# Performance work log

Measured on AMD Instinct MI355X. Metric: run time of the kernel, lower is better.

Reference implementation:

```python
import jax, jax.numpy as jnp
import numpy as np

S, B, E = 128, 64, 512          # seqlen, batch, incoming feature dim
P_LEN, P_DIM = 160, 512         # post length, post_size
H = 1024                        # hidden_size; GRU input_size = E + P_DIM = 1024
NEG = -1000000000.0             # masked_fill value in maskedSoftmax


def setup_inputs() -> dict:
    key = jax.random.key(0)
    ks = jax.random.split(key, 11)
    s = 1.0 / np.sqrt(H)
    u = lambda k, shp: jax.random.uniform(k, shp, jnp.float32, -s, s)
    return {
        "incoming": jax.random.normal(ks[0], (S, B, E), jnp.float32),
        "post": jax.random.normal(ks[1], (P_LEN, B, P_DIM), jnp.float32),
        "h_init": u(ks[2], (1, 1, H)),
        "weight_ih": u(ks[3], (3 * H, E + P_DIM)),
        "weight_hh": u(ks[4], (3 * H, H)),
        "bias_ih": u(ks[5], (3 * H,)),
        "bias_hh": u(ks[6], (3 * H,)),
        "wq": u(ks[7], (P_DIM, H)),
        "bq": u(ks[8], (P_DIM,)),
        "length": jax.random.randint(ks[9], (B,), 1, S + 1),
        "post_length": jax.random.randint(ks[10], (B,), 1, P_LEN + 1),
    }


def reference(incoming, post, h_init, weight_ih, weight_hh, bias_ih, bias_hh,
              wq, bq, length, post_length):
    seqlen, batch = incoming.shape[0], incoming.shape[1]
    plen = post.shape[0]
    h0 = jnp.broadcast_to(h_init[0], (batch, h_init.shape[-1]))  # h_init.repeat(1,B,1)[0]
    pos_mask = jnp.arange(plen)[:, None] < post_length[None, :]  # [P, B]

    def step(h, xt_i):
        xt, i = xt_i
        # attention over post, softmax along post-length axis (dim 0)
        query = h @ wq.T + bq                                   # [B, P_DIM]
        scores = jnp.einsum('pbd,bd->pb', post, query)          # [P, B]
        attn = jax.nn.softmax(jnp.where(pos_mask, scores, NEG), axis=0)
        context = jnp.einsum('pb,pbd->bd', attn, post)          # [B, P_DIM]
        x = jnp.concatenate([xt, context], axis=-1)             # [B, E + P_DIM]
        # torch GRUCell (gate order: r, z, n)
        gi = x @ weight_ih.T + bias_ih                          # [B, 3H]
        gh = h @ weight_hh.T + bias_hh                          # [B, 3H]
        i_r, i_z, i_n = jnp.split(gi, 3, axis=-1)
        h_r, h_z, h_n = jnp.split(gh, 3, axis=-1)
        r = jax.nn.sigmoid(i_r + h_r)
        z = jax.nn.sigmoid(i_z + h_z)
        n = jnp.tanh(i_n + r * h_n)
        h_new = (1.0 - z) * n + z * h
        # zero out finished sequences: h_now * (length > i)
        h_new = h_new * (length > i)[:, None].astype(h.dtype)
        return h_new, h_new

    h_last, hs = jax.lax.scan(step, h0, (incoming, jnp.arange(seqlen)))
    return hs, h_last
```

## Files before the change

kernel.cpp:

```cpp
#include <hip/hip_runtime.h>

#define S_LEN 128
#define BATCH 64
#define EDIM  512
#define PLEN  160
#define PDIM  512
#define HDIM  1024
#define G3    3072
#define NBLK  128
#define NTHR  256
#define PROWS 144

typedef _Float16 half8v  __attribute__((ext_vector_type(8)));
typedef _Float16 half4v  __attribute__((ext_vector_type(4)));
typedef _Float16 half2v  __attribute__((ext_vector_type(2)));
typedef float    f32x4   __attribute__((ext_vector_type(4)));

#define CTRL_UINTS 24576
#define OFF_CTRL ((size_t)0)
#define OFF_WIH  ((size_t)(CTRL_UINTS*4))
#define OFF_WHH  (OFF_WIH  + (size_t)G3*HDIM*2)
#define OFF_WQH  (OFF_WHH  + (size_t)G3*HDIM*2)
#define OFF_INC  (OFF_WQH  + (size_t)PDIM*HDIM*2)
#define OFF_POST (OFF_INC  + (size_t)S_LEN*BATCH*EDIM*2)
#define OFF_HH   (OFF_POST + (size_t)PLEN*BATCH*PDIM*2)
#define OFF_QH   (OFF_HH   + (size_t)BATCH*HDIM*2)
#define OFF_CTX  (OFF_QH   + (size_t)BATCH*PDIM*2)

__global__ void init_ctrl(unsigned* u) {
    int i = threadIdx.x + blockIdx.x * blockDim.x;
    if (i < CTRL_UINTS) u[i] = 0u;
}

__device__ __forceinline__ float wave_sum(float v) {
    v += __shfl_xor(v, 32); v += __shfl_xor(v, 16); v += __shfl_xor(v, 8);
    v += __shfl_xor(v, 4);  v += __shfl_xor(v, 2);  v += __shfl_xor(v, 1);
    return v;
}
__device__ __forceinline__ float wave_max(float v) {
    v = fmaxf(v, __shfl_xor(v, 32)); v = fmaxf(v, __shfl_xor(v, 16));
    v = fmaxf(v, __shfl_xor(v, 8));  v = fmaxf(v, __shfl_xor(v, 4));
    v = fmaxf(v, __shfl_xor(v, 2));  v = fmaxf(v, __shfl_xor(v, 1));
    return v;
}

__device__ __forceinline__ void gbar(unsigned* arrive, unsigned& gen, int tid, int blk) {
    gen++;
    __syncthreads();
    if (tid == 0)
        __hip_atomic_store(&arrive[blk * 32], gen, __ATOMIC_RELEASE, __HIP_MEMORY_SCOPE_AGENT);
    if (tid < NBLK) {
        unsigned* fl = &arrive[tid * 32];
        while (__hip_atomic_load(fl, __ATOMIC_RELAXED, __HIP_MEMORY_SCOPE_AGENT) < gen)
            __builtin_amdgcn_s_sleep(1);
        __hip_atomic_load(fl, __ATOMIC_ACQUIRE, __HIP_MEMORY_SCOPE_AGENT);
    }
    __syncthreads();
}

__device__ __forceinline__ void mfma_acc(f32x4& acc, const _Float16* __restrict__ A, int lda,
                                         const _Float16* __restrict__ Bb, int ldb,
                                         int ksteps, int lane) {
    const _Float16* ap = A  + (size_t)(lane & 15) * lda + ((lane >> 4) << 3);
    const _Float16* bp = Bb + (size_t)(lane & 15) * ldb + ((lane >> 4) << 3);
    #pragma unroll
    for (int ks = 0; ks < ksteps; ++ks) {
        half8v av = *(const half8v*)ap;
        half8v bv = *(const half8v*)bp;
        acc = __builtin_amdgcn_mfma_f32_16x16x32_f16(av, bv, acc, 0, 0, 0);
        ap += 32; bp += 32;
    }
}

__device__ __forceinline__ void mfma_acc3(f32x4& a0, f32x4& a1, f32x4& a2,
        const _Float16* __restrict__ A, int lda,
        const _Float16* __restrict__ B0, const _Float16* __restrict__ B1,
        const _Float16* __restrict__ B2, int ldb, int ksteps, int lane) {
    const _Float16* ap = A  + (size_t)(lane & 15) * lda + ((lane >> 4) << 3);
    const _Float16* p0 = B0 + (size_t)(lane & 15) * ldb + ((lane >> 4) << 3);
    const _Float16* p1 = B1 + (size_t)(lane & 15) * ldb + ((lane >> 4) << 3);
    const _Float16* p2 = B2 + (size_t)(lane & 15) * ldb + ((lane >> 4) << 3);
    #pragma unroll
    for (int ks = 0; ks < ksteps; ++ks) {
        half8v av = *(const half8v*)ap;
        a0 = __builtin_amdgcn_mfma_f32_16x16x32_f16(av, *(const half8v*)p0, a0, 0, 0, 0);
        a1 = __builtin_amdgcn_mfma_f32_16x16x32_f16(av, *(const half8v*)p1, a1, 0, 0, 0);
        a2 = __builtin_amdgcn_mfma_f32_16x16x32_f16(av, *(const half8v*)p2, a2, 0, 0, 0);
        ap += 32; p0 += 32; p1 += 32; p2 += 32;
    }
}

__global__ __launch_bounds__(NTHR, 1) void gru_main(
    const float* __restrict__ incoming, const float* __restrict__ post,
    const float* __restrict__ h_init,   const float* __restrict__ w_ih,
    const float* __restrict__ w_hh,     const float* __restrict__ b_ih,
    const float* __restrict__ b_hh,     const float* __restrict__ wq,
    const float* __restrict__ bq,       const int* __restrict__ length,
    const int* __restrict__ post_length, float* __restrict__ out,
    char* __restrict__ ws)
{
    const int tid  = threadIdx.x;
    const int blk  = blockIdx.x;
    const int lane = tid & 63;
    const int wv   = tid >> 6;

    unsigned* arrive = (unsigned*)(ws + OFF_CTRL);
    unsigned* qflag  = (unsigned*)(ws + OFF_CTRL) + 4096;
    _Float16* wih_h  = (_Float16*)(ws + OFF_WIH);
    _Float16* whh_h  = (_Float16*)(ws + OFF_WHH);
    _Float16* wq_h   = (_Float16*)(ws + OFF_WQH);
    _Float16* inc_h  = (_Float16*)(ws + OFF_INC);
    _Float16* post_h = (_Float16*)(ws + OFF_POST);
    _Float16* h_h    = (_Float16*)(ws + OFF_HH);
    _Float16* query_h= (_Float16*)(ws + OFF_QH);
    _Float16* ctx_h  = (_Float16*)(ws + OFF_CTX);

    __shared__ _Float16 s_post[PROWS * PDIM];
    __shared__ _Float16 s_q[PDIM];
    __shared__ float s_scores[PLEN];
    __shared__ float s_w[PLEN];
    __shared__ float s_bc[2];

    unsigned gen = 0;

    float bsr = 0.f, bsz = 0.f, bin_ = 0.f, bhn = 0.f, bqv = 0.f;
    float hp[4] = {0.f, 0.f, 0.f, 0.f};
    int lenb[4] = {0, 0, 0, 0};
    int j0 = 0, ab = 0, plen = 0;
    if (blk < 64) {
        j0 = blk * 16;
        const int j = j0 + (lane & 15);
        bsr  = b_ih[j] + b_hh[j];
        bsz  = b_ih[HDIM + j] + b_hh[HDIM + j];
        bin_ = b_ih[2*HDIM + j];
        bhn  = b_hh[2*HDIM + j];
        if (blk < 32) bqv = bq[blk*16 + (lane & 15)];
        const float hi = h_init[j];
        const int r0 = wv*16 + ((lane >> 4) << 2);
        #pragma unroll
        for (int r = 0; r < 4; ++r) { hp[r] = hi; lenb[r] = length[r0 + r]; }
    } else {
        ab = blk - 64;
        plen = post_length[ab];
    }

    {
        const int NV4_W    = G3*HDIM/4;
        const int NV4_WQ   = PDIM*HDIM/4;
        const int NV4_INC  = S_LEN*BATCH*EDIM/4;
        const int NV4_POST = PLEN*BATCH*PDIM/4;
        const int TOT = 2*NV4_W + NV4_WQ + NV4_INC + NV4_POST;
        for (int i = blk*NTHR + tid; i < TOT; i += NBLK*NTHR) {
            const float* s; _Float16* dp; int o;
            if (i < NV4_W)                          { s = w_ih;     dp = wih_h;  o = i; }
            else if (i < 2*NV4_W)                   { s = w_hh;     dp = whh_h;  o = i - NV4_W; }
            else if (i < 2*NV4_W + NV4_WQ)          { s = wq;       dp = wq_h;   o = i - 2*NV4_W; }
            else if (i < 2*NV4_W + NV4_WQ + NV4_INC){ s = incoming; dp = inc_h;  o = i - 2*NV4_W - NV4_WQ; }
            else                                    { s = post;     dp = post_h; o = i - 2*NV4_W - NV4_WQ - NV4_INC; }
            f32x4 v = *(const f32x4*)(s + (size_t)o*4);
            half4v hv4 = {(_Float16)v.x, (_Float16)v.y, (_Float16)v.z, (_Float16)v.w};
            *(half4v*)(dp + (size_t)o*4) = hv4;
        }
        for (int i = blk*NTHR + tid; i < BATCH*HDIM; i += NBLK*NTHR)
            h_h[i] = (_Float16)h_init[i & (HDIM-1)];
    }
    if (blk >= 64) {
        for (int i = tid; i < PROWS*PDIM; i += NTHR) {
            const int p = i >> 9, d = i & (PDIM-1);
            s_post[i] = (_Float16)post[((size_t)p*BATCH + ab)*PDIM + d];
        }
    }
    gbar(arrive, gen, tid, blk);

    for (int t = 0; t < S_LEN; ++t) {
        f32x4 ghr = {0.f,0.f,0.f,0.f}, ghz = {0.f,0.f,0.f,0.f}, ghn_ = {0.f,0.f,0.f,0.f};
        f32x4 gir = {0.f,0.f,0.f,0.f}, giz = {0.f,0.f,0.f,0.f}, gin_ = {0.f,0.f,0.f,0.f};

        if (blk < 64) {
            if (blk < 32) {
                const int q0 = blk * 16;
                f32x4 qa = {0.f,0.f,0.f,0.f};
                mfma_acc(qa, h_h + (size_t)(wv*16)*HDIM, HDIM,
                         wq_h + (size_t)q0*HDIM, HDIM, HDIM/32, lane);
                const int q  = q0 + (lane & 15);
                const int r0 = wv*16 + ((lane >> 4) << 2);
                #pragma unroll
                for (int r = 0; r < 4; ++r)
                    query_h[(size_t)(r0+r)*PDIM + q] = (_Float16)(qa[r] + bqv);
                __syncthreads();
                if (tid == 0)
                    __hip_atomic_store(&qflag[blk * 32], (unsigned)(t+1),
                                       __ATOMIC_RELEASE, __HIP_MEMORY_SCOPE_AGENT);
            }
            mfma_acc3(ghr, ghz, ghn_, h_h + (size_t)(wv*16)*HDIM, HDIM,
                      whh_h + (size_t)j0*HDIM,
                      whh_h + (size_t)(HDIM + j0)*HDIM,
                      whh_h + (size_t)(2*HDIM + j0)*HDIM, HDIM, HDIM/32, lane);
            mfma_acc3(gir, giz, gin_, inc_h + ((size_t)t*BATCH + wv*16)*EDIM, EDIM,
                      wih_h + (size_t)j0*HDIM,
                      wih_h + (size_t)(HDIM + j0)*HDIM,
                      wih_h + (size_t)(2*HDIM + j0)*HDIM, HDIM, EDIM/32, lane);
        } else {
            half8v srow[4];
            #pragma unroll
            for (int i = 0; i < 4; ++i)
                srow[i] = *(const half8v*)(post_h +
                            ((size_t)(PROWS + wv + 4*i)*BATCH + ab)*PDIM + lane*8);
            if (tid < 32) {
                unsigned* fl = &qflag[tid * 32];
                while (__hip_atomic_load(fl, __ATOMIC_RELAXED, __HIP_MEMORY_SCOPE_AGENT) < (unsigned)(t+1))
                    __builtin_amdgcn_s_sleep(1);
                __hip_atomic_load(fl, __ATOMIC_ACQUIRE, __HIP_MEMORY_SCOPE_AGENT);
            }
            __syncthreads();
            if (tid < PDIM/8)
                *(half8v*)&s_q[tid*8] = *(const half8v*)&query_h[(size_t)ab*PDIM + tid*8];
            __syncthreads();
            const half8v qv = *(const half8v*)&s_q[lane*8];
            #pragma unroll 2
            for (int p = wv; p < PROWS; p += 4) {
                const half8v pv = *(const half8v*)&s_post[(size_t)p*PDIM + lane*8];
                float sd = 0.f;
                #pragma unroll
                for (int jj = 0; jj < 8; ++jj) sd += (float)pv[jj] * (float)qv[jj];
                sd = wave_sum(sd);
                if (lane == 0) s_scores[p] = sd;
            }
            #pragma unroll
            for (int i = 0; i < 4; ++i) {
                const half8v pv = srow[i];
                float sd = 0.f;
                #pragma unroll
                for (int jj = 0; jj < 8; ++jj) sd += (float)pv[jj] * (float)qv[jj];
                sd = wave_sum(sd);
                if (lane == 0) s_scores[PROWS + wv + 4*i] = sd;
            }
            __syncthreads();
            if (wv == 0) {
                float m = -1e30f;
                for (int p = lane; p < plen; p += 64) m = fmaxf(m, s_scores[p]);
                m = wave_max(m);
                if (lane == 0) s_bc[0] = m;
            }
            __syncthreads();
            const float mx = s_bc[0];
            if (tid < PLEN) s_w[tid] = (tid < plen) ? __expf(s_scores[tid] - mx) : 0.f;
            __syncthreads();
            if (wv == 0) {
                float ss = 0.f;
                for (int p = lane; p < PLEN; p += 64) ss += s_w[p];
                ss = wave_sum(ss);
                if (lane == 0) s_bc[1] = 1.f / ss;
            }
            __syncthreads();
            const float inv_den = s_bc[1];
            const int d0 = tid << 1;
            float ca = 0.f, cb = 0.f;
            #pragma unroll 4
            for (int p = 0; p < PROWS; ++p) {
                const half2v pv2 = *(const half2v*)&s_post[(size_t)p*PDIM + d0];
                const float wp = s_w[p];
                ca += wp * (float)pv2[0];
                cb += wp * (float)pv2[1];
            }
            #pragma unroll 4
            for (int p = PROWS; p < PLEN; ++p) {
                const half2v pv2 = *(const half2v*)(post_h + ((size_t)p*BATCH + ab)*PDIM + d0);
                const float wp = s_w[p];
                ca += wp * (float)pv2[0];
                cb += wp * (float)pv2[1];
            }
            half2v cv; cv[0] = (_Float16)(ca * inv_den); cv[1] = (_Float16)(cb * inv_den);
            *(half2v*)&ctx_h[(size_t)ab*PDIM + d0] = cv;
        }
        gbar(arrive, gen, tid, blk);

        if (blk < 64) {
            mfma_acc3(gir, giz, gin_, ctx_h + (size_t)(wv*16)*PDIM, PDIM,
                      wih_h + (size_t)j0*HDIM + PDIM,
                      wih_h + (size_t)(HDIM + j0)*HDIM + PDIM,
                      wih_h + (size_t)(2*HDIM + j0)*HDIM + PDIM, HDIM, PDIM/32, lane);
            const int j  = j0 + (lane & 15);
            const int r0 = wv*16 + ((lane >> 4) << 2);
            #pragma unroll
            for (int r = 0; r < 4; ++r) {
                const int b = r0 + r;
                const float rg = 1.f / (1.f + __expf(-(gir[r] + ghr[r] + bsr)));
                const float zg = 1.f / (1.f + __expf(-(giz[r] + ghz[r] + bsz)));
                const float e2 = __expf(2.f * ((gin_[r] + bin_) + rg * (ghn_[r] + bhn)));
                const float ng = 1.f - 2.f / (e2 + 1.f);
                float hv = (1.f - zg) * ng + zg * hp[r];
                if (lenb[r] <= t) hv = 0.f;
                hp[r] = hv;
                out[(size_t)t*BATCH*HDIM + (size_t)b*HDIM + j] = hv;
                h_h[(size_t)b*HDIM + j] = (_Float16)hv;
                if (t == S_LEN - 1)
                    out[(size_t)S_LEN*BATCH*HDIM + (size_t)b*HDIM + j] = hv;
            }
        }
        if (t < S_LEN - 1) gbar(arrive, gen, tid, blk);
    }
}

extern "C" void kernel_launch(void* const* d_in, const int* in_sizes, int n_in,
                              void* d_out, int out_size, void* d_ws, size_t ws_size,
                              hipStream_t stream) {
    (void)in_sizes; (void)n_in; (void)out_size; (void)ws_size;
    const float* incoming    = (const float*)d_in[0];
    const float* post        = (const float*)d_in[1];
    const float* h_init      = (const float*)d_in[2];
    const float* w_ih        = (const float*)d_in[3];
    const float* w_hh        = (const float*)d_in[4];
    const float* b_ih        = (const float*)d_in[5];
    const float* b_hh        = (const float*)d_in[6];
    const float* wq          = (const float*)d_in[7];
    const float* bq          = (const float*)d_in[8];
    const int*   length      = (const int*)d_in[9];
    const int*   post_length = (const int*)d_in[10];
    float* out = (float*)d_out;

    init_ctrl<<<96, 256, 0, stream>>>((unsigned*)d_ws);
    gru_main<<<NBLK, NTHR, 0, stream>>>(incoming, post, h_init, w_ih, w_hh, b_ih, b_hh,
                                        wq, bq, length, post_length, out, (char*)d_ws);
}
```

Before: 5.818 ms.

## Replace global barriers with per-block flags and double-buffered hidden state

Replaces the two grid-wide barriers per timestep with producer/consumer flags: GRU blocks publish h into a double buffer and signal hflag, and attention blocks publish context and signal cflag. The query projection moves from GRU blocks 0-31 into each attention block, which computes the query for its own batch row from h staged in LDS. This shortens the recurrence critical path and removes one flag handoff. In exchange, each attention block redundantly reads the full Wq, and the flag waits use relaxed atomics without an explicit acquire, which could pose memory-ordering risks.

```diff
diff --git a/kernel.cpp b/kernel.cpp
--- a/kernel.cpp
+++ b/kernel.cpp
@@ -23,9 +23,8 @@
 #define OFF_WQH  (OFF_WHH  + (size_t)G3*HDIM*2)
 #define OFF_INC  (OFF_WQH  + (size_t)PDIM*HDIM*2)
 #define OFF_POST (OFF_INC  + (size_t)S_LEN*BATCH*EDIM*2)
-#define OFF_HH   (OFF_POST + (size_t)PLEN*BATCH*PDIM*2)
-#define OFF_QH   (OFF_HH   + (size_t)BATCH*HDIM*2)
-#define OFF_CTX  (OFF_QH   + (size_t)BATCH*PDIM*2)
+#define OFF_HB   (OFF_POST + (size_t)PLEN*BATCH*PDIM*2)
+#define OFF_CTX  (OFF_HB   + (size_t)2*BATCH*HDIM*2)
 
 __global__ void init_ctrl(unsigned* u) {
     int i = threadIdx.x + blockIdx.x * blockDim.x;
@@ -42,6 +41,21 @@
     v = fmaxf(v, __shfl_xor(v, 8));  v = fmaxf(v, __shfl_xor(v, 4));
     v = fmaxf(v, __shfl_xor(v, 2));  v = fmaxf(v, __shfl_xor(v, 1));
     return v;
+}
+
+__device__ __forceinline__ half8v ld16_coh(const _Float16* p) {
+    unsigned long long a = __hip_atomic_load((const unsigned long long*)p,
+                                             __ATOMIC_RELAXED, __HIP_MEMORY_SCOPE_AGENT);
+    unsigned long long b = __hip_atomic_load((const unsigned long long*)p + 1,
+                                             __ATOMIC_RELAXED, __HIP_MEMORY_SCOPE_AGENT);
+    union { unsigned long long u[2]; half8v v; } c;
+    c.u[0] = a; c.u[1] = b;
+    return c.v;
+}
+
+__device__ __forceinline__ void poll_ge(unsigned* fl, unsigned target) {
+    while (__hip_atomic_load(fl, __ATOMIC_RELAXED, __HIP_MEMORY_SCOPE_AGENT) < target)
+        __builtin_amdgcn_s_sleep(1);
 }
 
 __device__ __forceinline__ void gbar(unsigned* arrive, unsigned& gen, int tid, int blk) {
@@ -56,20 +70,6 @@
         __hip_atomic_load(fl, __ATOMIC_ACQUIRE, __HIP_MEMORY_SCOPE_AGENT);
     }
     __syncthreads();
-}
-
-__device__ __forceinline__ void mfma_acc(f32x4& acc, const _Float16* __restrict__ A, int lda,
-                                         const _Float16* __restrict__ Bb, int ldb,
-                                         int ksteps, int lane) {
-    const _Float16* ap = A  + (size_t)(lane & 15) * lda + ((lane >> 4) << 3);
-    const _Float16* bp = Bb + (size_t)(lane & 15) * ldb + ((lane >> 4) << 3);
-    #pragma unroll
-    for (int ks = 0; ks < ksteps; ++ks) {
-        half8v av = *(const half8v*)ap;
-        half8v bv = *(const half8v*)bp;
-        acc = __builtin_amdgcn_mfma_f32_16x16x32_f16(av, bv, acc, 0, 0, 0);
-        ap += 32; bp += 32;
-    }
 }
 
 __device__ __forceinline__ void mfma_acc3(f32x4& a0, f32x4& a1, f32x4& a2,
@@ -90,6 +90,24 @@
     }
 }
 
+__device__ __forceinline__ void mfma_acc3_coh(f32x4& a0, f32x4& a1, f32x4& a2,
+        const _Float16* A, int lda,
+        const _Float16* __restrict__ B0, const _Float16* __restrict__ B1,
+        const _Float16* __restrict__ B2, int ldb, int ksteps, int lane) {
+    const _Float16* ap = A  + (size_t)(lane & 15) * lda + ((lane >> 4) << 3);
+    const _Float16* p0 = B0 + (size_t)(lane & 15) * ldb + ((lane >> 4) << 3);
+    const _Float16* p1 = B1 + (size_t)(lane & 15) * ldb + ((lane >> 4) << 3);
+    const _Float16* p2 = B2 + (size_t)(lane & 15) * ldb + ((lane >> 4) << 3);
+    #pragma unroll
+    for (int ks = 0; ks < ksteps; ++ks) {
+        half8v av = ld16_coh(ap);
+        a0 = __builtin_amdgcn_mfma_f32_16x16x32_f16(av, *(const half8v*)p0, a0, 0, 0, 0);
+        a1 = __builtin_amdgcn_mfma_f32_16x16x32_f16(av, *(const half8v*)p1, a1, 0, 0, 0);
+        a2 = __builtin_amdgcn_mfma_f32_16x16x32_f16(av, *(const half8v*)p2, a2, 0, 0, 0);
+        ap += 32; p0 += 32; p1 += 32; p2 += 32;
+    }
+}
+
 __global__ __launch_bounds__(NTHR, 1) void gru_main(
     const float* __restrict__ incoming, const float* __restrict__ post,
     const float* __restrict__ h_init,   const float* __restrict__ w_ih,
@@ -104,26 +122,28 @@
     const int lane = tid & 63;
     const int wv   = tid >> 6;
 
-    unsigned* arrive = (unsigned*)(ws + OFF_CTRL);
-    unsigned* qflag  = (unsigned*)(ws + OFF_CTRL) + 4096;
+    unsigned* hflag  = (unsigned*)(ws + OFF_CTRL);
+    unsigned* cflag  = (unsigned*)(ws + OFF_CTRL) + 2048;
+    unsigned* arrive = (unsigned*)(ws + OFF_CTRL) + 4096;
     _Float16* wih_h  = (_Float16*)(ws + OFF_WIH);
     _Float16* whh_h  = (_Float16*)(ws + OFF_WHH);
     _Float16* wq_h   = (_Float16*)(ws + OFF_WQH);
     _Float16* inc_h  = (_Float16*)(ws + OFF_INC);
     _Float16* post_h = (_Float16*)(ws + OFF_POST);
-    _Float16* h_h    = (_Float16*)(ws + OFF_HH);
-    _Float16* query_h= (_Float16*)(ws + OFF_QH);
+    _Float16* hb     = (_Float16*)(ws + OFF_HB);
     _Float16* ctx_h  = (_Float16*)(ws + OFF_CTX);
 
-    __shared__ _Float16 s_post[PROWS * PDIM];
-    __shared__ _Float16 s_q[PDIM];
+    __shared__ __align__(16) _Float16 s_post[PROWS * PDIM];
+    __shared__ __align__(16) _Float16 s_h[HDIM];
+    __shared__ __align__(16) _Float16 s_q[PDIM];
     __shared__ float s_scores[PLEN];
     __shared__ float s_w[PLEN];
     __shared__ float s_bc[2];
 
     unsigned gen = 0;
 
-    float bsr = 0.f, bsz = 0.f, bin_ = 0.f, bhn = 0.f, bqv = 0.f;
+    float bsr = 0.f, bsz = 0.f, bin_ = 0.f, bhn = 0.f;
+    float bq_[8] = {0.f,0.f,0.f,0.f,0.f,0.f,0.f,0.f};
     float hp[4] = {0.f, 0.f, 0.f, 0.f};
     int lenb[4] = {0, 0, 0, 0};
     int j0 = 0, ab = 0, plen = 0;
@@ -134,7 +154,6 @@
         bsz  = b_ih[HDIM + j] + b_hh[HDIM + j];
         bin_ = b_ih[2*HDIM + j];
         bhn  = b_hh[2*HDIM + j];
-        if (blk < 32) bqv = bq[blk*16 + (lane & 15)];
         const float hi = h_init[j];
         const int r0 = wv*16 + ((lane >> 4) << 2);
         #pragma unroll
@@ -142,6 +161,8 @@
     } else {
         ab = blk - 64;
         plen = post_length[ab];
+        #pragma unroll
+        for (int i = 0; i < 8; ++i) bq_[i] = bq[wv*128 + i*16 + (lane & 15)];
     }
 
     {
@@ -162,7 +183,7 @@
             *(half4v*)(dp + (size_t)o*4) = hv4;
         }
         for (int i = blk*NTHR + tid; i < BATCH*HDIM; i += NBLK*NTHR)
-            h_h[i] = (_Float16)h_init[i & (HDIM-1)];
+            hb[i] = (_Float16)h_init[i & (HDIM-1)];
     }
     if (blk >= 64) {
         for (int i = tid; i < PROWS*PDIM; i += NTHR) {
@@ -172,114 +193,32 @@
     }
     gbar(arrive, gen, tid, blk);
 
-    for (int t = 0; t < S_LEN; ++t) {
-        f32x4 ghr = {0.f,0.f,0.f,0.f}, ghz = {0.f,0.f,0.f,0.f}, ghn_ = {0.f,0.f,0.f,0.f};
-        f32x4 gir = {0.f,0.f,0.f,0.f}, giz = {0.f,0.f,0.f,0.f}, gin_ = {0.f,0.f,0.f,0.f};
-
-        if (blk < 64) {
-            if (blk < 32) {
-                const int q0 = blk * 16;
-                f32x4 qa = {0.f,0.f,0.f,0.f};
-                mfma_acc(qa, h_h + (size_t)(wv*16)*HDIM, HDIM,
-                         wq_h + (size_t)q0*HDIM, HDIM, HDIM/32, lane);
-                const int q  = q0 + (lane & 15);
-                const int r0 = wv*16 + ((lane >> 4) << 2);
-                #pragma unroll
-                for (int r = 0; r < 4; ++r)
-                    query_h[(size_t)(r0+r)*PDIM + q] = (_Float16)(qa[r] + bqv);
-                __syncthreads();
-                if (tid == 0)
-                    __hip_atomic_store(&qflag[blk * 32], (unsigned)(t+1),
-                                       __ATOMIC_RELEASE, __HIP_MEMORY_SCOPE_AGENT);
-            }
-            mfma_acc3(ghr, ghz, ghn_, h_h + (size_t)(wv*16)*HDIM, HDIM,
-                      whh_h + (size_t)j0*HDIM,
-                      whh_h + (size_t)(HDIM + j0)*HDIM,
-                      whh_h + (size_t)(2*HDIM + j0)*HDIM, HDIM, HDIM/32, lane);
+    if (blk < 64) {
+        for (int t = 0; t < S_LEN; ++t) {
+            if (tid < 64) poll_ge(&hflag[tid * 32], (unsigned)t);
+            __syncthreads();
+            const _Float16* hin = hb + (size_t)(t & 1) * BATCH * HDIM;
+
+            f32x4 ghr = {0.f,0.f,0.f,0.f}, ghz = {0.f,0.f,0.f,0.f}, ghn_ = {0.f,0.f,0.f,0.f};
+            f32x4 gir = {0.f,0.f,0.f,0.f}, giz = {0.f,0.f,0.f,0.f}, gin_ = {0.f,0.f,0.f,0.f};
+            mfma_acc3_coh(ghr, ghz, ghn_, hin + (size_t)(wv*16)*HDIM, HDIM,
+                          whh_h + (size_t)j0*HDIM,
+                          whh_h + (size_t)(HDIM + j0)*HDIM,
+                          whh_h + (size_t)(2*HDIM + j0)*HDIM, HDIM, HDIM/32, lane);
             mfma_acc3(gir, giz, gin_, inc_h + ((size_t)t*BATCH + wv*16)*EDIM, EDIM,
                       wih_h + (size_t)j0*HDIM,
                       wih_h + (size_t)(HDIM + j0)*HDIM,
                       wih_h + (size_t)(2*HDIM + j0)*HDIM, HDIM, EDIM/32, lane);
-        } else {
-            half8v srow[4];
-            #pragma unroll
-            for (int i = 0; i < 4; ++i)
-                srow[i] = *(const half8v*)(post_h +
-                            ((size_t)(PROWS + wv + 4*i)*BATCH + ab)*PDIM + lane*8);
-            if (tid < 32) {
-                unsigned* fl = &qflag[tid * 32];
-                while (__hip_atomic_load(fl, __ATOMIC_RELAXED, __HIP_MEMORY_SCOPE_AGENT) < (unsigned)(t+1))
-                    __builtin_amdgcn_s_sleep(1);
-                __hip_atomic_load(fl, __ATOMIC_ACQUIRE, __HIP_MEMORY_SCOPE_AGENT);
-            }
-            __syncthreads();
-            if (tid < PDIM/8)
-                *(half8v*)&s_q[tid*8] = *(const half8v*)&query_h[(size_t)ab*PDIM + tid*8];
-            __syncthreads();
-            const half8v qv = *(const half8v*)&s_q[lane*8];
-            #pragma unroll 2
-            for (int p = wv; p < PROWS; p += 4) {
-                const half8v pv = *(const half8v*)&s_post[(size_t)p*PDIM + lane*8];
-                float sd = 0.f;
-                #pragma unroll
-                for (int jj = 0; jj < 8; ++jj) sd += (float)pv[jj] * (float)qv[jj];
-                sd = wave_sum(sd);
-                if (lane == 0) s_scores[p] = sd;
-            }
-            #pragma unroll
-            for (int i = 0; i < 4; ++i) {
-                const half8v pv = srow[i];
-                float sd = 0.f;
-                #pragma unroll
-                for (int jj = 0; jj < 8; ++jj) sd += (float)pv[jj] * (float)qv[jj];
-                sd = wave_sum(sd);
-                if (lane == 0) s_scores[PROWS + wv + 4*i] = sd;
-            }
-            __syncthreads();
-            if (wv == 0) {
-                float m = -1e30f;
-                for (int p = lane; p < plen; p += 64) m = fmaxf(m, s_scores[p]);
-                m = wave_max(m);
-                if (lane == 0) s_bc[0] = m;
-            }
-            __syncthreads();
-            const float mx = s_bc[0];
-            if (tid < PLEN) s_w[tid] = (tid < plen) ? __expf(s_scores[tid] - mx) : 0.f;
-            __syncthreads();
-            if (wv == 0) {
-                float ss = 0.f;
-                for (int p = lane; p < PLEN; p += 64) ss += s_w[p];
-                ss = wave_sum(ss);
-                if (lane == 0) s_bc[1] = 1.f / ss;
-            }
-            __syncthreads();
-            const float inv_den = s_bc[1];
-            const int d0 = tid << 1;
-            float ca = 0.f, cb = 0.f;
-            #pragma unroll 4
-            for (int p = 0; p < PROWS; ++p) {
-                const half2v pv2 = *(const half2v*)&s_post[(size_t)p*PDIM + d0];
-                const float wp = s_w[p];
-                ca += wp * (float)pv2[0];
-                cb += wp * (float)pv2[1];
-            }
-            #pragma unroll 4
-            for (int p = PROWS; p < PLEN; ++p) {
-                const half2v pv2 = *(const half2v*)(post_h + ((size_t)p*BATCH + ab)*PDIM + d0);
-                const float wp = s_w[p];
-                ca += wp * (float)pv2[0];
-                cb += wp * (float)pv2[1];
-            }
-            half2v cv; cv[0] = (_Float16)(ca * inv_den); cv[1] = (_Float16)(cb * inv_den);
-            *(half2v*)&ctx_h[(size_t)ab*PDIM + d0] = cv;
-        }
-        gbar(arrive, gen, tid, blk);
-
-        if (blk < 64) {
-            mfma_acc3(gir, giz, gin_, ctx_h + (size_t)(wv*16)*PDIM, PDIM,
-                      wih_h + (size_t)j0*HDIM + PDIM,
-                      wih_h + (size_t)(HDIM + j0)*HDIM + PDIM,
-                      wih_h + (size_t)(2*HDIM + j0)*HDIM + PDIM, HDIM, PDIM/32, lane);
+
+            if (tid < 64) poll_ge(&cflag[tid * 32], (unsigned)(t + 1));
+            __syncthreads();
+
+            mfma_acc3_coh(gir, giz, gin_, ctx_h + (size_t)(wv*16)*PDIM, PDIM,
+                          wih_h + (size_t)j0*HDIM + PDIM,
+                          wih_h + (size_t)(HDIM + j0)*HDIM + PDIM,
+                          wih_h + (size_t)(2*HDIM + j0)*HDIM + PDIM, HDIM, PDIM/32, lane);
+
+            _Float16* hout = hb + (size_t)((t + 1) & 1) * BATCH * HDIM;
             const int j  = j0 + (lane & 15);
             const int r0 = wv*16 + ((lane >> 4) << 2);
             #pragma unroll
@@ -293,12 +232,116 @@
                 if (lenb[r] <= t) hv = 0.f;
                 hp[r] = hv;
                 out[(size_t)t*BATCH*HDIM + (size_t)b*HDIM + j] = hv;
-                h_h[(size_t)b*HDIM + j] = (_Float16)hv;
+                hout[(size_t)b*HDIM + j] = (_Float16)hv;
                 if (t == S_LEN - 1)
                     out[(size_t)S_LEN*BATCH*HDIM + (size_t)b*HDIM + j] = hv;
             }
+            __syncthreads();
+            if (tid == 0)
+                __hip_atomic_store(&hflag[blk * 32], (unsigned)(t + 1),
+                                   __ATOMIC_RELEASE, __HIP_MEMORY_SCOPE_AGENT);
         }
-        if (t < S_LEN - 1) gbar(arrive, gen, tid, blk);
+    } else {
+        for (int t = 0; t < S_LEN; ++t) {
+            half8v srow[4];
+            #pragma unroll
+            for (int i = 0; i < 4; ++i)
+                srow[i] = *(const half8v*)(post_h +
+                            ((size_t)(PROWS + wv + 4*i)*BATCH + ab)*PDIM + lane*8);
+
+            if (tid < 64) poll_ge(&hflag[tid * 32], (unsigned)t);
+            __syncthreads();
+            {
+                const unsigned long long* hin =
+                    (const unsigned long long*)(hb + (size_t)(t & 1)*BATCH*HDIM + (size_t)ab*HDIM);
+                ((unsigned long long*)s_h)[tid] =
+                    __hip_atomic_load(hin + tid, __ATOMIC_RELAXED, __HIP_MEMORY_SCOPE_AGENT);
+            }
+            __syncthreads();
+
+            {
+                f32x4 qa[8] = {{0.f,0.f,0.f,0.f},{0.f,0.f,0.f,0.f},{0.f,0.f,0.f,0.f},{0.f,0.f,0.f,0.f},
+                               {0.f,0.f,0.f,0.f},{0.f,0.f,0.f,0.f},{0.f,0.f,0.f,0.f},{0.f,0.f,0.f,0.f}};
+                const int ko = (lane >> 4) << 3;
+                const _Float16* bb = wq_h + ((size_t)(wv*128) + (lane & 15))*HDIM + ko;
+                #pragma unroll 4
+                for (int ks = 0; ks < 32; ++ks) {
+                    const half8v av = *(const half8v*)(s_h + ko + ks*32);
+                    #pragma unroll
+                    for (int i = 0; i < 8; ++i)
+                        qa[i] = __builtin_amdgcn_mfma_f32_16x16x32_f16(av,
+                                    *(const half8v*)(bb + (size_t)i*16*HDIM + ks*32), qa[i], 0, 0, 0);
+                }
+                if (lane < 16) {
+                    #pragma unroll
+                    for (int i = 0; i < 8; ++i)
+                        s_q[wv*128 + i*16 + lane] = (_Float16)(qa[i][0] + bq_[i]);
+                }
+            }
+            __syncthreads();
+
+            const half8v qv = *(const half8v*)&s_q[lane*8];
+            #pragma unroll 2
+            for (int p = wv; p < PROWS; p += 4) {
+                const half8v pv = *(const half8v*)&s_post[(size_t)p*PDIM + lane*8];
+                float sd = 0.f;
+                #pragma unroll
+                for (int jj = 0; jj < 8; ++jj) sd += (float)pv[jj] * (float)qv[jj];
+                sd = wave_sum(sd);
+                if (lane == 0) s_scores[p] = sd;
+            }
+            #pragma unroll
+            for (int i = 0; i < 4; ++i) {
+                const half8v pv = srow[i];
+                float sd = 0.f;
+                #pragma unroll
+                for (int jj = 0; jj < 8; ++jj) sd += (float)pv[jj] * (float)qv[jj];
+                sd = wave_sum(sd);
+                if (lane == 0) s_scores[PROWS + wv + 4*i] = sd;
+            }
+            __syncthreads();
+            if (wv == 0) {
+                float m = -1e30f;
+                for (int p = lane; p < plen; p += 64) m = fmaxf(m, s_scores[p]);
+                m = wave_max(m);
+                if (lane == 0) s_bc[0] = m;
+            }
+            __syncthreads();
+            const float mx = s_bc[0];
+            if (tid < PLEN) s_w[tid] = (tid < plen) ? __expf(s_scores[tid] - mx) : 0.f;
+            __syncthreads();
+            if (wv == 0) {
+                float ss = 0.f;
+                for (int p = lane; p < PLEN; p += 64) ss += s_w[p];
+                ss = wave_sum(ss);
+                if (lane == 0) s_bc[1] = 1.f / ss;
+            }
+            __syncthreads();
+            const float inv_den = s_bc[1];
+            const int d0 = tid << 1;
+            float ca = 0.f, cb = 0.f;
+            #pragma unroll 4
+            for (int p = 0; p < PROWS; ++p) {
+                const half2v pv2 = *(const half2v*)&s_post[(size_t)p*PDIM + d0];
+                const float wp = s_w[p];
+                ca += wp * (float)pv2[0];
+                cb += wp * (float)pv2[1];
+            }
+            #pragma unroll 4
+            for (int p = PROWS; p < PLEN; ++p) {
+                const half2v pv2 = *(const half2v*)(post_h + ((size_t)p*BATCH + ab)*PDIM + d0);
+                const float wp = s_w[p];
+                ca += wp * (float)pv2[0];
+                cb += wp * (float)pv2[1];
+            }
+            half2v cv; cv[0] = (_Float16)(ca * inv_den); cv[1] = (_Float16)(cb * inv_den);
+            *(half2v*)&ctx_h[(size_t)ab*PDIM + d0] = cv;
+
+            __syncthreads();
+            if (tid == 0)
+                __hip_atomic_store(&cflag[ab * 32], (unsigned)(t + 1),
+                                   __ATOMIC_RELEASE, __HIP_MEMORY_SCOPE_AGENT);
+        }
     }
 }
 
```

Measured after the change: 7.627 ms. 1.31x slower.
